# Optimization experiments

Hardware: AMD Instinct MI355X
Metric: run time of the kernel (lower is better)

## Reference

```python
import jax, jax.numpy as jnp
import numpy as np

EPS = 1e-5
DIM_HEAD = 64
HEADS = 8

def layernorm(x, gamma, beta):
    mu = jnp.mean(x, axis=-1, keepdims=True)
    var = jnp.var(x, axis=-1, keepdims=True)
    return (x - mu) * jax.lax.rsqrt(var + EPS) * gamma + beta

def setup_inputs() -> dict:
    key = jax.random.key(0)
    ks = jax.random.split(key, 8)
    b, n, dh = 1, 896, 3072       # batch, enformer seq len, enformer_hidden_dim
    c, j, dc = 64, 127, 1024      # num contexts (tracks), context len, context_dim
    inner = HEADS * DIM_HEAD      # 512
    return {
        "embeddings": jax.random.normal(ks[0], (b, n, dh), jnp.float32),
        "context": jax.random.normal(ks[1], (c, j, dc), jnp.float32),
        "context_mask": jax.random.randint(ks[2], (b, j), 0, 2) > 0,
        "q_gamma": jnp.ones((dh,), jnp.float32),
        "q_beta": jnp.zeros((dh,), jnp.float32),
        "kv_gamma": jnp.ones((dc,), jnp.float32),
        "kv_beta": jnp.zeros((dc,), jnp.float32),
        "Wq": jax.random.normal(ks[3], (dh, inner), jnp.float32) * 0.02,
        "Wkv": jax.random.normal(ks[4], (dc, 2 * inner), jnp.float32) * 0.02,
        "null_k": jax.random.normal(ks[5], (inner,), jnp.float32),
        "null_v": jax.random.normal(ks[6], (inner,), jnp.float32),
        "Wo": jax.random.normal(ks[7], (inner, dh), jnp.float32) * 0.02,
        "bo": jnp.zeros((dh,), jnp.float32),
        "Wp": jax.random.normal(jax.random.fold_in(key, 9), (dh, 1), jnp.float32) * 0.02,
        "bp": jnp.zeros((1,), jnp.float32),
    }

def reference(embeddings, context, context_mask, q_gamma, q_beta, kv_gamma, kv_beta,
              Wq, Wkv, null_k, null_v, Wo, bo, Wp, bp):
    h, d = HEADS, DIM_HEAD
    scale = d ** -0.5
    b, n, dh = embeddings.shape
    c = context.shape[0]
    # projections
    q = layernorm(embeddings, q_gamma, q_beta) @ Wq            # (b, n, h*d)
    kv = layernorm(context, kv_gamma, kv_beta) @ Wkv           # (c, j, 2*h*d)
    k, v = jnp.split(kv, 2, axis=-1)
    # prepend null key/value token
    k = jnp.concatenate([jnp.broadcast_to(null_k, (c, 1, h * d)), k], axis=1)
    v = jnp.concatenate([jnp.broadcast_to(null_v, (c, 1, h * d)), v], axis=1)
    # split heads: (b, h, i, d) / (c, h, j, d)
    q = q.reshape(b, n, h, d).transpose(0, 2, 1, 3)
    k = k.reshape(c, -1, h, d).transpose(0, 2, 1, 3)
    v = v.reshape(c, -1, h, d).transpose(0, 2, 1, 3)
    sim = jnp.einsum('bhid,chjd->bchij', q, k) * scale         # (b, c, h, i, j+1)
    # mask: pad with True for the null token, broadcast over c, h, i
    mask = jnp.pad(context_mask, ((0, 0), (1, 0)), constant_values=True)
    sim = jnp.where(mask[:, None, None, None, :], sim, -jnp.finfo(sim.dtype).max)
    attn = jax.nn.softmax(sim, axis=-1)
    out = jnp.einsum('bchij,chjd->bchid', attn, v)             # (b, c, h, i, d)
    out = out.transpose(0, 1, 3, 2, 4).reshape(b, c, n, h * d)  # (b, c, n, h*d)
    branch = out @ Wo + bo                                     # (b, c, n, dh)
    emb = embeddings[:, None] + branch                         # (b, c, n, dh)
    pred = jax.nn.softplus((emb @ Wp + bp)[..., 0])            # (b, c, n)
    return pred.transpose(0, 2, 1)                             # (b, n, c)
```

## Files before the change

kernel.cpp:

```cpp
#include <hip/hip_runtime.h>
#include <math.h>

#define N_SEQ   896
#define DH      3072
#define NCTX    64
#define JLEN    127
#define DC      1024
#define HEADS   8
#define DHEAD   64
#define INNER   512
#define MKV     8128
#define MKVPAD  8192

typedef __bf16 bf16x8 __attribute__((ext_vector_type(8)));
typedef float  f32x4  __attribute__((ext_vector_type(4)));

#define OFF_EDOT   0LL
#define OFF_QBF    (OFF_EDOT + N_SEQ)
#define OFF_KBF    (OFF_QBF  + (long long)N_SEQ*INNER/2)
#define OFF_VPM    (OFF_KBF  + (long long)NCTX*128*INNER/2)
#define OFF_VPNULL (OFF_VPM  + (long long)MKV*8)
#define OFF_WOP    (OFF_VPNULL + 8)
#define OFF_BOP    (OFF_WOP  + INNER)
#define OFF_SBUF   (OFF_BOP  + 16)
#define OFF_ANQ    (OFF_SBUF + (long long)NCTX*HEADS*N_SEQ)
#define OFF_ANKV   (OFF_ANQ  + (long long)N_SEQ*DH/2)
#define OFF_WQT    (OFF_ANKV + (long long)MKVPAD*DC/2)
#define OFF_WKT    (OFF_WQT  + (long long)INNER*DH/2)
#define OFF_WVPT   (OFF_WKT  + (long long)INNER*DC/2)
#define OFF_QSL    (OFF_WVPT + 16*1024/2)

__device__ __forceinline__ void async_copy16(const __bf16* g, __bf16* l) {
    __builtin_amdgcn_global_load_lds(
        (const __attribute__((address_space(1))) unsigned int*)g,
        (__attribute__((address_space(3))) unsigned int*)l,
        16, 0, 0);
}

#define A_BOP  512
#define A_MISC 513
#define A_T0   514
#define GRIDA  (A_T0 + 2048)

__global__ __launch_bounds__(256)
void prep_a_kernel(const float* __restrict__ Wq, const float* __restrict__ Wkv,
                   const float* __restrict__ Wo, const float* __restrict__ bo,
                   const float* __restrict__ Wp, const float* __restrict__ nullk,
                   __bf16* __restrict__ WQT, __bf16* __restrict__ WKT,
                   __bf16* __restrict__ WVPT, float* __restrict__ WOP,
                   float* __restrict__ BOP, __bf16* __restrict__ KBF)
{
    __shared__ float tT[32][33];
    const int bid = blockIdx.x, tid = threadIdx.x;
    const int lane = tid & 63, wid = tid >> 6;

    if (bid < 512) {
        const float* worow = Wo + (long long)bid * DH;
        float s = 0.f;
        #pragma unroll
        for (int c = 0; c < 3; ++c) {
            int col = c * 1024 + tid * 4;
            float4 a = *(const float4*)&worow[col];
            float4 w = *(const float4*)&Wp[col];
            s += a.x*w.x + a.y*w.y + a.z*w.z + a.w*w.w;
        }
        #pragma unroll
        for (int o = 1; o < 64; o <<= 1) s += __shfl_xor(s, o);
        float* red = &tT[0][0];
        if (lane == 0) red[wid] = s;
        __syncthreads();
        if (tid == 0) WOP[bid] = red[0] + red[1] + red[2] + red[3];
    } else if (bid == A_BOP) {
        float* red = &tT[0][0];
        float s = 0.f;
        #pragma unroll
        for (int i = 0; i < 3; ++i) {
            int k = i * 1024 + tid * 4;
            float4 a = *(const float4*)&bo[k];
            float4 w = *(const float4*)&Wp[k];
            s += a.x*w.x + a.y*w.y + a.z*w.z + a.w*w.w;
        }
        #pragma unroll
        for (int o = 1; o < 64; o <<= 1) s += __shfl_xor(s, o);
        if (lane == 0) red[wid] = s;
        __syncthreads();
        if (tid == 0) *BOP = red[0] + red[1] + red[2] + red[3];
    } else if (bid == A_MISC) {
        for (int i = tid; i < 8 * 1024; i += 256)
            WVPT[8 * 1024 + i] = (__bf16)0.f;
        for (int i = tid; i < NCTX * INNER; i += 256) {
            int c = i >> 9, d2 = i & 511;
            KBF[(long long)(c * 128) * INNER + d2] = (__bf16)nullk[d2];
        }
    } else {
        int t = bid - A_T0;
        const float* src; __bf16* dst; int srcS, dstS, rb, cb;
        if (t < 1536) {
            rb = (t >> 4) * 32; cb = (t & 15) * 32;
            src = Wq; srcS = INNER; dst = WQT; dstS = DH;
        } else {
            int bi = t - 1536;
            rb = (bi >> 4) * 32; cb = (bi & 15) * 32;
            src = Wkv; srcS = 2 * INNER; dst = WKT; dstS = DC;
        }
        int tx = tid & 31, ty = tid >> 5;
        #pragma unroll
        for (int i = 0; i < 32; i += 8)
            tT[ty + i][tx] = src[(long long)(rb + ty + i) * srcS + cb + tx];
        __syncthreads();
        #pragma unroll
        for (int i = 0; i < 32; i += 8)
            dst[(long long)(cb + ty + i) * dstS + rb + tx] = (__bf16)tT[tx][ty + i];
    }
}

#define B_VPN  32
#define B_KV0  33
#define B_Q0   (B_KV0 + 2032)
#define GRIDB  (B_Q0 + 224)

__global__ __launch_bounds__(256)
void prep_b_kernel(const float* __restrict__ emb, const float* __restrict__ ctx,
                   const float* __restrict__ qg, const float* __restrict__ qb_,
                   const float* __restrict__ kvg, const float* __restrict__ kvb,
                   const float* __restrict__ Wp, const float* __restrict__ Wkv,
                   const float* __restrict__ nullv, const float* __restrict__ WOP,
                   __bf16* __restrict__ ANQ, __bf16* __restrict__ ANKV,
                   __bf16* __restrict__ WVPT, float* __restrict__ VPNULL,
                   float* __restrict__ EDOT)
{
    __shared__ float wsh[512];
    const int bid = blockIdx.x, tid = threadIdx.x;
    const int lane = tid & 63, wid = tid >> 6;

    if (bid < 32) {
        wsh[tid] = WOP[tid];
        wsh[tid + 256] = WOP[tid + 256];
        __syncthreads();
        int t = bid * 256 + tid;
        int k = t >> 3, h = t & 7;
        const float* src = Wkv + (long long)k * (2 * INNER) + INNER + h * 64;
        const float* wv = &wsh[h * 64];
        float s = 0.f;
        #pragma unroll
        for (int d2 = 0; d2 < 64; d2 += 4) {
            float4 a = *(const float4*)&src[d2];
            s += a.x*wv[d2] + a.y*wv[d2+1] + a.z*wv[d2+2] + a.w*wv[d2+3];
        }
        WVPT[h * 1024 + k] = (__bf16)s;
    } else if (bid == B_VPN) {
        wsh[tid] = WOP[tid];
        wsh[tid + 256] = WOP[tid + 256];
        __syncthreads();
        if (tid < 8) {
            int h = tid;
            float s = 0.f;
            #pragma unroll 16
            for (int d = 0; d < 64; ++d) s += nullv[h * 64 + d] * wsh[h * 64 + d];
            VPNULL[h] = s;
        }
    } else if (bid < B_Q0) {
        int r = (bid - B_KV0) * 4 + wid;
        const float* x = ctx + (long long)r * DC;
        f32x4 xv[4];
        float s = 0.f, ss = 0.f;
        #pragma unroll
        for (int c = 0; c < 4; ++c) {
            const f32x4* p = (const f32x4*)&x[c * 256 + lane * 4];
            xv[c] = __builtin_nontemporal_load(p);
            s  += xv[c][0] + xv[c][1] + xv[c][2] + xv[c][3];
            ss += xv[c][0]*xv[c][0] + xv[c][1]*xv[c][1]
                + xv[c][2]*xv[c][2] + xv[c][3]*xv[c][3];
        }
        #pragma unroll
        for (int o = 1; o < 64; o <<= 1) { s += __shfl_xor(s, o); ss += __shfl_xor(ss, o); }
        float m  = s * (1.f / DC);
        float rs = rsqrtf(ss * (1.f / DC) - m * m + 1e-5f);
        __bf16* op = ANKV + (long long)r * DC;
        #pragma unroll
        for (int c = 0; c < 4; ++c) {
            int col = c * 256 + lane * 4;
            float4 g4 = *(const float4*)&kvg[col];
            float4 b4 = *(const float4*)&kvb[col];
            __bf16 ov[4];
            ov[0] = (__bf16)((xv[c][0] - m) * rs * g4.x + b4.x);
            ov[1] = (__bf16)((xv[c][1] - m) * rs * g4.y + b4.y);
            ov[2] = (__bf16)((xv[c][2] - m) * rs * g4.z + b4.z);
            ov[3] = (__bf16)((xv[c][3] - m) * rs * g4.w + b4.w);
            *(ushort4*)&op[col] = *(ushort4*)ov;
        }
    } else {
        int r = (bid - B_Q0) * 4 + wid;
        const float* x = emb + (long long)r * DH;
        float s = 0.f, ss = 0.f, dp = 0.f;
        #pragma unroll
        for (int c = 0; c < 12; ++c) {
            int col = c * 256 + lane * 4;
            float4 a = *(const float4*)&x[col];
            float4 w = *(const float4*)&Wp[col];
            s  += a.x + a.y + a.z + a.w;
            ss += a.x*a.x + a.y*a.y + a.z*a.z + a.w*a.w;
            dp += a.x*w.x + a.y*w.y + a.z*w.z + a.w*w.w;
        }
        #pragma unroll
        for (int o = 1; o < 64; o <<= 1) {
            s += __shfl_xor(s, o); ss += __shfl_xor(ss, o); dp += __shfl_xor(dp, o);
        }
        float m  = s * (1.f / DH);
        float rs = rsqrtf(ss * (1.f / DH) - m * m + 1e-5f);
        __bf16* op = ANQ + (long long)r * DH;
        #pragma unroll
        for (int c = 0; c < 12; ++c) {
            int col = c * 256 + lane * 4;
            float4 a  = *(const float4*)&x[col];
            float4 g4 = *(const float4*)&qg[col];
            float4 b4 = *(const float4*)&qb_[col];
            __bf16 ov[4];
            ov[0] = (__bf16)((a.x - m) * rs * g4.x + b4.x);
            ov[1] = (__bf16)((a.y - m) * rs * g4.y + b4.y);
            ov[2] = (__bf16)((a.z - m) * rs * g4.z + b4.z);
            ov[3] = (__bf16)((a.w - m) * rs * g4.w + b4.w);
            *(ushort4*)&op[col] = *(ushort4*)ov;
        }
        if (lane == 0) EDOT[r] = dp;
    }
}

__global__ __launch_bounds__(256)
void proj_kernel(const __bf16* __restrict__ ANQ, const __bf16* __restrict__ WQT,
                 const __bf16* __restrict__ ANKV, const __bf16* __restrict__ WKT,
                 const __bf16* __restrict__ WVPT,
                 float* __restrict__ qsl, __bf16* __restrict__ kout,
                 float* __restrict__ vpm) {
    __shared__ __align__(16) __bf16 As[128 * 32];
    __shared__ __align__(16) __bf16 Bs[128 * 32];
    int b = blockIdx.x;
    int tid = threadIdx.x;
    int lane = tid & 63, w = tid >> 6;
    int n16 = lane & 15, quad = lane >> 4;
    int wr = (w >> 1) * 64, wc = (w & 1) * 64;

    const __bf16 *A, *B;
    int K, kbeg, kend, mode, slice = 0;
    long long m0, n0;
    if (b < 224) {
        mode = 0; slice = b / 28;
        int rem = b % 28;
        m0 = (long long)(rem % 7) * 128;
        n0 = (long long)(rem / 7) * 128;
        K = DH; kbeg = slice * 384; kend = kbeg + 384;
        A = ANQ; B = WQT;
    } else {
        mode = 1;
        int b2 = b - 224;
        m0 = (long long)(b2 & 63) * 128;
        n0 = (long long)(b2 >> 6) * 128;
        K = DC; kbeg = 0; kend = DC;
        A = ANKV; B = WKT;
    }
    bool dovp = (mode == 1) && (n0 == 0);

    const __bf16* aG = A + (m0 + (tid >> 2)) * K + (tid & 3) * 8;
    const __bf16* bG = B + (n0 + (tid >> 2)) * K + (tid & 3) * 8;
    __bf16* aL = As + tid * 8;
    __bf16* bL = Bs + tid * 8;

    f32x4 acc[4][4], accv[4];
    const f32x4 z = {0.f, 0.f, 0.f, 0.f};
    #pragma unroll
    for (int i = 0; i < 4; ++i) {
        accv[i] = z;
        #pragma unroll
        for (int j = 0; j < 4; ++j) acc[i][j] = z;
    }

    for (int k0 = kbeg; k0 < kend; k0 += 32) {
        async_copy16(aG + k0, aL);
        async_copy16(aG + (long long)64 * K + k0, aL + 2048);
        async_copy16(bG + k0, bL);
        async_copy16(bG + (long long)64 * K + k0, bL + 2048);
        bf16x8 bv;
        if (dovp) bv = *(const bf16x8*)&WVPT[n16 * 1024 + k0 + quad * 8];
        __syncthreads();
        bf16x8 af[4], bfr[4];
        #pragma unroll
        for (int i = 0; i < 4; ++i)
            af[i]  = *(const bf16x8*)&As[(wr + i * 16 + n16) * 32 + quad * 8];
        #pragma unroll
        for (int j = 0; j < 4; ++j)
            bfr[j] = *(const bf16x8*)&Bs[(wc + j * 16 + n16) * 32 + quad * 8];
        #pragma unroll
        for (int i = 0; i < 4; ++i)
            #pragma unroll
            for (int j = 0; j < 4; ++j)
                acc[i][j] = __builtin_amdgcn_mfma_f32_16x16x32_bf16(af[i], bfr[j], acc[i][j], 0, 0, 0);
        if (dovp) {
            #pragma unroll
            for (int i = 0; i < 4; ++i)
                accv[i] = __builtin_amdgcn_mfma_f32_16x16x32_bf16(af[i], bv, accv[i], 0, 0, 0);
        }
        __syncthreads();
    }

    if (mode == 0) {
        float* qdst = qsl + (long long)slice * (N_SEQ * INNER);
        #pragma unroll
        for (int i = 0; i < 4; ++i)
            #pragma unroll
            for (int r = 0; r < 4; ++r) {
                long long gr = m0 + wr + i * 16 + quad * 4 + r;
                #pragma unroll
                for (int j = 0; j < 4; ++j) {
                    long long gc = n0 + wc + j * 16 + n16;
                    qdst[gr * INNER + gc] = acc[i][j][r];
                }
            }
    } else {
        #pragma unroll
        for (int i = 0; i < 4; ++i)
            #pragma unroll
            for (int r = 0; r < 4; ++r) {
                long long gr = m0 + wr + i * 16 + quad * 4 + r;
                if (gr >= MKV) continue;
                int cc = (int)(gr / JLEN), jj = (int)(gr % JLEN);
                #pragma unroll
                for (int j = 0; j < 4; ++j) {
                    long long gc = n0 + wc + j * 16 + n16;
                    kout[((long long)(cc * 128) + jj + 1) * INNER + gc] = (__bf16)acc[i][j][r];
                }
                if (dovp && n16 < 8) vpm[gr * 8 + n16] = accv[i][r];
            }
    }
}

__global__ __launch_bounds__(256)
void qreduce_kernel(const float* __restrict__ qsl, __bf16* __restrict__ qbf) {
    int i = blockIdx.x * 256 + threadIdx.x;
    float4 s4 = {0.f, 0.f, 0.f, 0.f};
    #pragma unroll
    for (int k = 0; k < 8; ++k) {
        float4 a = *(const float4*)&qsl[(long long)k * (N_SEQ * INNER) + i * 4];
        s4.x += a.x; s4.y += a.y; s4.z += a.z; s4.w += a.w;
    }
    __bf16 ov[4] = {(__bf16)s4.x, (__bf16)s4.y, (__bf16)s4.z, (__bf16)s4.w};
    *(ushort4*)&qbf[i * 4] = *(ushort4*)ov;
}

#define KROW 72

__global__ __launch_bounds__(256)
void attn_mfma_kernel(const __bf16* __restrict__ qb, const __bf16* __restrict__ kb,
                      const float* __restrict__ vpm, const float* __restrict__ vpnull,
                      const int* __restrict__ mask, float* __restrict__ s_buf) {
    __shared__ __align__(16) __bf16 ksh[128 * KROW];
    __shared__ float vpsh[128];
    __shared__ float amsh[128];
    int ch = blockIdx.x;
    int h = ch & 7, c = ch >> 3;
    int tid = threadIdx.x;
    int lane = tid & 63, w = tid >> 6;
    int n16 = lane & 15, quad = lane >> 4;

    const __bf16* kbase = kb + (long long)(c * 128) * INNER + h * DHEAD;
    #pragma unroll
    for (int p = 0; p < 4; ++p) {
        int chunk = tid + p * 256;
        int row = chunk >> 3, o = chunk & 7;
        bf16x8 v = *(const bf16x8*)(kbase + (long long)row * INNER + o * 8);
        *(bf16x8*)&ksh[row * KROW + o * 8] = v;
    }
    if (tid < 128) {
        vpsh[tid] = (tid == 0) ? vpnull[h] : vpm[(long long)(c * JLEN + tid - 1) * 8 + h];
        amsh[tid] = (tid == 0) ? 0.f : (mask[tid - 1] ? 0.f : -3.0e38f);
    }
    __syncthreads();

    bf16x8 bF[8][2];
    #pragma unroll
    for (int t = 0; t < 8; ++t)
        #pragma unroll
        for (int s = 0; s < 2; ++s)
            bF[t][s] = *(const bf16x8*)&ksh[(t * 16 + n16) * KROW + s * 32 + quad * 8];

    float vpv[8], am[8];
    #pragma unroll
    for (int t = 0; t < 8; ++t) {
        vpv[t] = vpsh[t * 16 + n16];
        am[t]  = amsh[t * 16 + n16];
    }

    const __bf16* qbase = qb + h * DHEAD;
    const f32x4 zero = {0.f, 0.f, 0.f, 0.f};

    for (int xi = 0; xi < 7; ++xi) {
        bf16x8 aF[2][2];
        int r0s[2];
        #pragma unroll
        for (int it2 = 0; it2 < 2; ++it2) {
            int tile = xi * 8 + it2 * 4 + w;
            r0s[it2] = tile * 16;
            const __bf16* qrow = qbase + (long long)(r0s[it2] + n16) * INNER + quad * 8;
            aF[it2][0] = *(const bf16x8*)(qrow);
            aF[it2][1] = *(const bf16x8*)(qrow + 32);
        }

        #pragma unroll
        for (int it2 = 0; it2 < 2; ++it2) {
            int r0 = r0s[it2];
            f32x4 acc[8];
            #pragma unroll
            for (int t = 0; t < 8; ++t) {
                acc[t] = __builtin_amdgcn_mfma_f32_16x16x32_bf16(aF[it2][0], bF[t][0], zero,   0, 0, 0);
                acc[t] = __builtin_amdgcn_mfma_f32_16x16x32_bf16(aF[it2][1], bF[t][1], acc[t], 0, 0, 0);
            }
            float mloc = -3.0e38f;
            #pragma unroll
            for (int t = 0; t < 8; ++t)
                #pragma unroll
                for (int r = 0; r < 4; ++r)
                    mloc = fmaxf(mloc, acc[t][r] * 0.125f + am[t]);
            #pragma unroll
            for (int o = 1; o < 16; o <<= 1) mloc = fmaxf(mloc, __shfl_xor(mloc, o, 16));
            float lr[4] = {0.f, 0.f, 0.f, 0.f}, pr[4] = {0.f, 0.f, 0.f, 0.f};
            #pragma unroll
            for (int t = 0; t < 8; ++t) {
                #pragma unroll
                for (int r = 0; r < 4; ++r) {
                    float e = __expf(acc[t][r] * 0.125f + am[t] - mloc);
                    lr[r] += e; pr[r] += e * vpv[t];
                }
            }
            #pragma unroll
            for (int o = 1; o < 16; o <<= 1) {
                #pragma unroll
                for (int r = 0; r < 4; ++r) {
                    lr[r] += __shfl_xor(lr[r], o, 16);
                    pr[r] += __shfl_xor(pr[r], o, 16);
                }
            }
            if (n16 == 0) {
                #pragma unroll
                for (int r = 0; r < 4; ++r)
                    s_buf[(long long)ch * N_SEQ + r0 + quad * 4 + r] = pr[r] / lr[r];
            }
        }
    }
}

__global__ void final_kernel(const float* __restrict__ s_buf,
                             const float* __restrict__ e_dot,
                             const float* __restrict__ bop,
                             const float* __restrict__ bp,
                             float* __restrict__ out) {
    int t = blockIdx.x * blockDim.x + threadIdx.x;
    if (t >= N_SEQ * NCTX) return;
    int n = t >> 6, c = t & 63;
    float s = 0.f;
    #pragma unroll
    for (int h = 0; h < HEADS; ++h) s += s_buf[((long long)(c * HEADS + h)) * N_SEQ + n];
    float x = e_dot[n] + s + *bop + *bp;
    out[t] = fmaxf(x, 0.f) + log1pf(__expf(-fabsf(x)));
}

extern "C" void kernel_launch(void* const* d_in, const int* in_sizes, int n_in,
                              void* d_out, int out_size, void* d_ws, size_t ws_size,
                              hipStream_t stream) {
    const float* emb   = (const float*)d_in[0];
    const float* ctx   = (const float*)d_in[1];
    const int*   cmask = (const int*)  d_in[2];
    const float* qg    = (const float*)d_in[3];
    const float* qb_   = (const float*)d_in[4];
    const float* kvg   = (const float*)d_in[5];
    const float* kvb   = (const float*)d_in[6];
    const float* Wq    = (const float*)d_in[7];
    const float* Wkv   = (const float*)d_in[8];
    const float* nullk = (const float*)d_in[9];
    const float* nullv = (const float*)d_in[10];
    const float* Wo    = (const float*)d_in[11];
    const float* bo    = (const float*)d_in[12];
    const float* Wp    = (const float*)d_in[13];
    const float* bp    = (const float*)d_in[14];
    float* out  = (float*)d_out;
    float* ws_f = (float*)d_ws;

    float*  EDOT   = ws_f + OFF_EDOT;
    __bf16* QBF    = (__bf16*)(ws_f + OFF_QBF);
    __bf16* KBF    = (__bf16*)(ws_f + OFF_KBF);
    float*  VPM    = ws_f + OFF_VPM;
    float*  VPNULL = ws_f + OFF_VPNULL;
    float*  WOP    = ws_f + OFF_WOP;
    float*  BOP    = ws_f + OFF_BOP;
    float*  SBUF   = ws_f + OFF_SBUF;
    __bf16* ANQ    = (__bf16*)(ws_f + OFF_ANQ);
    __bf16* ANKV   = (__bf16*)(ws_f + OFF_ANKV);
    __bf16* WQT    = (__bf16*)(ws_f + OFF_WQT);
    __bf16* WKT    = (__bf16*)(ws_f + OFF_WKT);
    __bf16* WVPT   = (__bf16*)(ws_f + OFF_WVPT);
    float*  QSL    = ws_f + OFF_QSL;

    prep_a_kernel<<<GRIDA, 256, 0, stream>>>(
        Wq, Wkv, Wo, bo, Wp, nullk, WQT, WKT, WVPT, WOP, BOP, KBF);
    prep_b_kernel<<<GRIDB, 256, 0, stream>>>(
        emb, ctx, qg, qb_, kvg, kvb, Wp, Wkv, nullv, WOP,
        ANQ, ANKV, WVPT, VPNULL, EDOT);
    proj_kernel<<<480, 256, 0, stream>>>(ANQ, WQT, ANKV, WKT, WVPT, QSL, KBF, VPM);
    qreduce_kernel<<<(N_SEQ * INNER) / 1024, 256, 0, stream>>>(QSL, QBF);
    attn_mfma_kernel<<<NCTX * HEADS, 256, 0, stream>>>(
        QBF, KBF, VPM, VPNULL, cmask, SBUF);
    final_kernel<<<(N_SEQ * NCTX + 255) / 256, 256, 0, stream>>>(SBUF, EDOT, BOP, bp, out);
}
```

Before: 219.3 us.

## Fuse split-K Q reduction and final softplus into producers via last-block atomics

Removes the separate qreduce and final kernels. In proj_kernel, the last of eight split-K slice blocks for each Q tile, detected with an atomic counter, sums the slices and writes the bf16 Q. In attn_mfma_kernel, the last head block for each context sums the per-head results and applies softplus. This saves two kernel launches and their inter-kernel gaps. In exchange it adds threadfences, atomics and serialized tail work on the last-arriving blocks.

Result: slower. 312.7 us (+42.6%).

```diff
diff --git a/kernel.cpp b/kernel.cpp
--- a/kernel.cpp
+++ b/kernel.cpp
@@ -29,6 +29,7 @@
 #define OFF_WKT    (OFF_WQT  + (long long)INNER*DH/2)
 #define OFF_WVPT   (OFF_WKT  + (long long)INNER*DC/2)
 #define OFF_QSL    (OFF_WVPT + 16*1024/2)
+#define OFF_CNT    (OFF_QSL  + (long long)8*N_SEQ*INNER)
 
 __device__ __forceinline__ void async_copy16(const __bf16* g, __bf16* l) {
     __builtin_amdgcn_global_load_lds(
@@ -48,7 +49,8 @@
                    const float* __restrict__ Wp, const float* __restrict__ nullk,
                    __bf16* __restrict__ WQT, __bf16* __restrict__ WKT,
                    __bf16* __restrict__ WVPT, float* __restrict__ WOP,
-                   float* __restrict__ BOP, __bf16* __restrict__ KBF)
+                   float* __restrict__ BOP, __bf16* __restrict__ KBF,
+                   int* __restrict__ CNT)
 {
     __shared__ float tT[32][33];
     const int bid = blockIdx.x, tid = threadIdx.x;
@@ -86,6 +88,7 @@
         __syncthreads();
         if (tid == 0) *BOP = red[0] + red[1] + red[2] + red[3];
     } else if (bid == A_MISC) {
+        if (tid < 92) CNT[tid] = 0;
         for (int i = tid; i < 8 * 1024; i += 256)
             WVPT[8 * 1024 + i] = (__bf16)0.f;
         for (int i = tid; i < NCTX * INNER; i += 256) {
@@ -231,9 +234,11 @@
                  const __bf16* __restrict__ ANKV, const __bf16* __restrict__ WKT,
                  const __bf16* __restrict__ WVPT,
                  float* __restrict__ qsl, __bf16* __restrict__ kout,
-                 float* __restrict__ vpm) {
+                 float* __restrict__ vpm, __bf16* __restrict__ qbf,
+                 int* __restrict__ cntQ) {
     __shared__ __align__(16) __bf16 As[128 * 32];
     __shared__ __align__(16) __bf16 Bs[128 * 32];
+    __shared__ int sOld;
     int b = blockIdx.x;
     int tid = threadIdx.x;
     int lane = tid & 63, w = tid >> 6;
@@ -241,11 +246,11 @@
     int wr = (w >> 1) * 64, wc = (w & 1) * 64;
 
     const __bf16 *A, *B;
-    int K, kbeg, kend, mode, slice = 0;
+    int K, kbeg, kend, mode, slice = 0, rem = 0;
     long long m0, n0;
     if (b < 224) {
         mode = 0; slice = b / 28;
-        int rem = b % 28;
+        rem = b % 28;
         m0 = (long long)(rem % 7) * 128;
         n0 = (long long)(rem / 7) * 128;
         K = DH; kbeg = slice * 384; kend = kbeg + 384;
@@ -315,6 +320,24 @@
                     qdst[gr * INNER + gc] = acc[i][j][r];
                 }
             }
+        __threadfence();
+        if (tid == 0) sOld = atomicAdd(&cntQ[rem], 1);
+        __syncthreads();
+        if (sOld == 7) {
+            __threadfence();
+            for (int idx = tid; idx < 128 * 32; idx += 256) {
+                long long gr = m0 + (idx >> 5);
+                long long gc = n0 + (idx & 31) * 4;
+                float4 s4 = {0.f, 0.f, 0.f, 0.f};
+                #pragma unroll
+                for (int k = 0; k < 8; ++k) {
+                    float4 a = *(const float4*)&qsl[(long long)k * (N_SEQ * INNER) + gr * INNER + gc];
+                    s4.x += a.x; s4.y += a.y; s4.z += a.z; s4.w += a.w;
+                }
+                __bf16 ov[4] = {(__bf16)s4.x, (__bf16)s4.y, (__bf16)s4.z, (__bf16)s4.w};
+                *(ushort4*)&qbf[gr * INNER + gc] = *(ushort4*)ov;
+            }
+        }
     } else {
         #pragma unroll
         for (int i = 0; i < 4; ++i)
@@ -333,28 +356,19 @@
     }
 }
 
-__global__ __launch_bounds__(256)
-void qreduce_kernel(const float* __restrict__ qsl, __bf16* __restrict__ qbf) {
-    int i = blockIdx.x * 256 + threadIdx.x;
-    float4 s4 = {0.f, 0.f, 0.f, 0.f};
-    #pragma unroll
-    for (int k = 0; k < 8; ++k) {
-        float4 a = *(const float4*)&qsl[(long long)k * (N_SEQ * INNER) + i * 4];
-        s4.x += a.x; s4.y += a.y; s4.z += a.z; s4.w += a.w;
-    }
-    __bf16 ov[4] = {(__bf16)s4.x, (__bf16)s4.y, (__bf16)s4.z, (__bf16)s4.w};
-    *(ushort4*)&qbf[i * 4] = *(ushort4*)ov;
-}
-
 #define KROW 72
 
 __global__ __launch_bounds__(256)
 void attn_mfma_kernel(const __bf16* __restrict__ qb, const __bf16* __restrict__ kb,
                       const float* __restrict__ vpm, const float* __restrict__ vpnull,
-                      const int* __restrict__ mask, float* __restrict__ s_buf) {
+                      const int* __restrict__ mask, float* __restrict__ s_buf,
+                      const float* __restrict__ e_dot, const float* __restrict__ bop,
+                      const float* __restrict__ bp, float* __restrict__ out,
+                      int* __restrict__ cntC) {
     __shared__ __align__(16) __bf16 ksh[128 * KROW];
     __shared__ float vpsh[128];
     __shared__ float amsh[128];
+    __shared__ int sOld;
     int ch = blockIdx.x;
     int h = ch & 7, c = ch >> 3;
     int tid = threadIdx.x;
@@ -445,21 +459,22 @@
             }
         }
     }
-}
-
-__global__ void final_kernel(const float* __restrict__ s_buf,
-                             const float* __restrict__ e_dot,
-                             const float* __restrict__ bop,
-                             const float* __restrict__ bp,
-                             float* __restrict__ out) {
-    int t = blockIdx.x * blockDim.x + threadIdx.x;
-    if (t >= N_SEQ * NCTX) return;
-    int n = t >> 6, c = t & 63;
-    float s = 0.f;
-    #pragma unroll
-    for (int h = 0; h < HEADS; ++h) s += s_buf[((long long)(c * HEADS + h)) * N_SEQ + n];
-    float x = e_dot[n] + s + *bop + *bp;
-    out[t] = fmaxf(x, 0.f) + log1pf(__expf(-fabsf(x)));
+
+    __threadfence();
+    if (tid == 0) sOld = atomicAdd(&cntC[c], 1);
+    __syncthreads();
+    if (sOld == 7) {
+        __threadfence();
+        float bsum = *bop + *bp;
+        for (int n = tid; n < N_SEQ; n += 256) {
+            float s = 0.f;
+            #pragma unroll
+            for (int hh = 0; hh < 8; ++hh)
+                s += s_buf[((long long)(c * HEADS + hh)) * N_SEQ + n];
+            float x = e_dot[n] + s + bsum;
+            out[n * NCTX + c] = fmaxf(x, 0.f) + log1pf(__expf(-fabsf(x)));
+        }
+    }
 }
 
 extern "C" void kernel_launch(void* const* d_in, const int* in_sizes, int n_in,
@@ -497,15 +512,15 @@
     __bf16* WKT    = (__bf16*)(ws_f + OFF_WKT);
     __bf16* WVPT   = (__bf16*)(ws_f + OFF_WVPT);
     float*  QSL    = ws_f + OFF_QSL;
+    int*    CNT    = (int*)(ws_f + OFF_CNT);
 
     prep_a_kernel<<<GRIDA, 256, 0, stream>>>(
-        Wq, Wkv, Wo, bo, Wp, nullk, WQT, WKT, WVPT, WOP, BOP, KBF);
+        Wq, Wkv, Wo, bo, Wp, nullk, WQT, WKT, WVPT, WOP, BOP, KBF, CNT);
     prep_b_kernel<<<GRIDB, 256, 0, stream>>>(
         emb, ctx, qg, qb_, kvg, kvb, Wp, Wkv, nullv, WOP,
         ANQ, ANKV, WVPT, VPNULL, EDOT);
-    proj_kernel<<<480, 256, 0, stream>>>(ANQ, WQT, ANKV, WKT, WVPT, QSL, KBF, VPM);
-    qreduce_kernel<<<(N_SEQ * INNER) / 1024, 256, 0, stream>>>(QSL, QBF);
+    proj_kernel<<<480, 256, 0, stream>>>(
+        ANQ, WQT, ANKV, WKT, WVPT, QSL, KBF, VPM, QBF, CNT);
     attn_mfma_kernel<<<NCTX * HEADS, 256, 0, stream>>>(
-        QBF, KBF, VPM, VPNULL, cmask, SBUF);
-    final_kernel<<<(N_SEQ * NCTX + 255) / 256, 256, 0, stream>>>(SBUF, EDOT, BOP, bp, out);
+        QBF, KBF, VPM, VPNULL, cmask, SBUF, EDOT, BOP, bp, out, CNT + 28);
 }
```
